# Performance work log

Measured on AMD Instinct MI355X. Metric: run time of the kernel, lower is better.

## Reference

```python
import jax, jax.numpy as jnp
import numpy as np

B, N, K = 128, 1000, 10  # queries, docs per query, NDCG cutoff (hard-coded k=10 in module)


def setup_inputs() -> dict:
    key = jax.random.key(0)
    k1, k2 = jax.random.split(key)
    predictions = jax.random.normal(k1, (B, N), dtype=jnp.float32)
    labels = jax.random.randint(k2, (B, N), 0, 5).astype(jnp.float32)  # graded relevance 0..4
    return {"predictions": predictions, "labels": labels}


def _ndcg_loss(predictions, rel, k=K):
    # relevance gathered in descending-score order, top-k only
    order = jnp.argsort(-predictions, axis=-1)[:, :k]            # [B, k]
    rel_by_score = jnp.take_along_axis(rel, order, axis=-1)      # [B, k]
    ideal_rel, _ = jax.lax.top_k(rel, k)                          # [B, k] sorted desc
    denoms = jnp.log2(jnp.arange(k, dtype=jnp.float32) + 2.0)    # [k]
    dcg = jnp.sum(rel_by_score / denoms, axis=-1)                # [B]
    idcg = jnp.sum(ideal_rel / denoms, axis=-1)                  # [B]
    return jnp.sum(1.0 - dcg / idcg)


def reference(predictions, labels):
    rel = jnp.power(2.0, labels) - 1.0
    return _ndcg_loss(predictions, rel)
```

## Files before the change

kernel.cpp:

```cpp
#include <hip/hip_runtime.h>
#include <stdint.h>

#define B_QUERIES 128
#define N_DOCS    1000
#define K_TOP     10
#define PER_LANE  16

__device__ __forceinline__ uint32_t f32_sortable(float f) {
    uint32_t u = __float_as_uint(f);
    return (u & 0x80000000u) ? ~u : (u | 0x80000000u);
}

__global__ __launch_bounds__(64) void ndcg_row_kernel(
        const float* __restrict__ pred,
        const float* __restrict__ lab,
        float* __restrict__ row_loss) {
    const int row  = blockIdx.x;
    const int lane = threadIdx.x;
    const float* p = pred + row * N_DOCS;
    const float* l = lab  + row * N_DOCS;

    __shared__ int s_lab[N_DOCS];

    const float denom[K_TOP] = {
        1.0f, 1.5849625f, 2.0f, 2.3219281f, 2.5849626f,
        2.8073549f, 3.0f, 3.1699250f, 3.3219281f, 3.4594316f
    };

    uint64_t key[PER_LANE];
    int hist[5] = {0, 0, 0, 0, 0};
    #pragma unroll
    for (int j = 0; j < PER_LANE; ++j) {
        int idx = lane + j * 64;
        if (idx < N_DOCS) {
            float pv = p[idx];
            key[j] = ((uint64_t)f32_sortable(pv) << 32) | (uint32_t)(~idx);
            int lv = (int)(l[idx] + 0.5f);
            s_lab[idx] = lv;
            hist[lv]++;
        } else {
            key[j] = 0;
        }
    }
    __syncthreads();

    #pragma unroll
    for (int v = 0; v < 5; ++v) {
        int h = hist[v];
        #pragma unroll
        for (int off = 32; off > 0; off >>= 1) h += __shfl_xor(h, off, 64);
        hist[v] = h;
    }

    uint64_t lastKey = ~0ull;
    float dcg = 0.0f;
    for (int r = 0; r < K_TOP; ++r) {
        uint64_t best = 0;
        #pragma unroll
        for (int j = 0; j < PER_LANE; ++j) {
            uint64_t k = key[j];
            if (k < lastKey && k > best) best = k;
        }
        #pragma unroll
        for (int off = 32; off > 0; off >>= 1) {
            uint64_t o = (uint64_t)__shfl_xor((unsigned long long)best, off, 64);
            if (o > best) best = o;
        }
        lastKey = best;
        int idx = (int)(~(uint32_t)(best & 0xFFFFFFFFu));
        int lv  = s_lab[idx];
        dcg += (float)((1 << lv) - 1) / denom[r];
    }

    float idcg = 0.0f;
    int pos = 0;
    for (int v = 4; v >= 1; --v) {
        int c = hist[v];
        float rel = (float)((1 << v) - 1);
        for (int t = 0; t < c && pos < K_TOP; ++t) {
            idcg += rel / denom[pos];
            ++pos;
        }
        if (pos >= K_TOP) break;
    }

    if (lane == 0) row_loss[row] = 1.0f - dcg / idcg;
}

__global__ __launch_bounds__(64) void ndcg_reduce_kernel(
        const float* __restrict__ row_loss, float* __restrict__ out) {
    int lane = threadIdx.x;
    float s = row_loss[lane] + row_loss[lane + 64];
    #pragma unroll
    for (int off = 32; off > 0; off >>= 1) s += __shfl_xor(s, off, 64);
    if (lane == 0) out[0] = s;
}

extern "C" void kernel_launch(void* const* d_in, const int* in_sizes, int n_in,
                              void* d_out, int out_size, void* d_ws, size_t ws_size,
                              hipStream_t stream) {
    (void)in_sizes; (void)n_in; (void)out_size; (void)ws_size;
    const float* pred = (const float*)d_in[0];
    const float* lab  = (const float*)d_in[1];
    float* out = (float*)d_out;
    float* ws  = (float*)d_ws;

    ndcg_row_kernel<<<B_QUERIES, 64, 0, stream>>>(pred, lab, ws);
    ndcg_reduce_kernel<<<1, 64, 0, stream>>>(ws, out);
}
```

Baseline: 69.03 us.

## Pack label into sort key, vectorize loads, tree-reduce top-k selection

```diff
diff --git a/kernel.cpp b/kernel.cpp
--- a/kernel.cpp
+++ b/kernel.cpp
@@ -3,12 +3,16 @@
 
 #define B_QUERIES 128
 #define N_DOCS    1000
+#define NVEC      250
 #define K_TOP     10
-#define PER_LANE  16
 
 __device__ __forceinline__ uint32_t f32_sortable(float f) {
     uint32_t u = __float_as_uint(f);
     return (u & 0x80000000u) ? ~u : (u | 0x80000000u);
+}
+
+__device__ __forceinline__ uint64_t u64max(uint64_t a, uint64_t b) {
+    return a > b ? a : b;
 }
 
 __global__ __launch_bounds__(64) void ndcg_row_kernel(
@@ -17,71 +21,78 @@
         float* __restrict__ row_loss) {
     const int row  = blockIdx.x;
     const int lane = threadIdx.x;
-    const float* p = pred + row * N_DOCS;
-    const float* l = lab  + row * N_DOCS;
+    const float4* p4 = (const float4*)(pred + row * N_DOCS);
+    const float4* l4 = (const float4*)(lab  + row * N_DOCS);
 
-    __shared__ int s_lab[N_DOCS];
-
-    const float denom[K_TOP] = {
-        1.0f, 1.5849625f, 2.0f, 2.3219281f, 2.5849626f,
-        2.8073549f, 3.0f, 3.1699250f, 3.3219281f, 3.4594316f
+    const float inv_denom[K_TOP] = {
+        1.0f, 0.63092977f, 0.5f, 0.43067656f, 0.38685282f,
+        0.35620719f, 0.33333334f, 0.31546488f, 0.30102998f, 0.28906483f
     };
 
-    uint64_t key[PER_LANE];
-    int hist[5] = {0, 0, 0, 0, 0};
+    uint64_t key[16];
+    uint64_t h = 0;
+
     #pragma unroll
-    for (int j = 0; j < PER_LANE; ++j) {
-        int idx = lane + j * 64;
-        if (idx < N_DOCS) {
-            float pv = p[idx];
-            key[j] = ((uint64_t)f32_sortable(pv) << 32) | (uint32_t)(~idx);
-            int lv = (int)(l[idx] + 0.5f);
-            s_lab[idx] = lv;
-            hist[lv]++;
-        } else {
-            key[j] = 0;
+    for (int j = 0; j < 4; ++j) {
+        int v = lane + j * 64;
+        bool act = (v < NVEC);
+        float4 pv = act ? p4[v] : make_float4(0.f, 0.f, 0.f, 0.f);
+        float4 lv = act ? l4[v] : make_float4(0.f, 0.f, 0.f, 0.f);
+        float pp[4] = {pv.x, pv.y, pv.z, pv.w};
+        float ll[4] = {lv.x, lv.y, lv.z, lv.w};
+        #pragma unroll
+        for (int c = 0; c < 4; ++c) {
+            int idx = v * 4 + c;
+            int li  = (int)(ll[c] + 0.5f);
+            uint64_t k = ((uint64_t)f32_sortable(pp[c]) << 32)
+                       | ((uint32_t)(1023 - idx) << 8)
+                       | (uint32_t)li;
+            key[j * 4 + c] = act ? k : 0ull;
+            if (act && li > 0) h += 1ull << ((li - 1) * 16);
         }
     }
-    __syncthreads();
 
     #pragma unroll
-    for (int v = 0; v < 5; ++v) {
-        int h = hist[v];
+    for (int off = 32; off > 0; off >>= 1)
+        h += (uint64_t)__shfl_xor((unsigned long long)h, off, 64);
+
+    float idcg = 0.0f;
+    {
+        int pos = 0;
         #pragma unroll
-        for (int off = 32; off > 0; off >>= 1) h += __shfl_xor(h, off, 64);
-        hist[v] = h;
+        for (int v = 4; v >= 1; --v) {
+            int c = (int)((h >> ((v - 1) * 16)) & 0xFFFFull);
+            float rel = (float)((1 << v) - 1);
+            while (c-- > 0 && pos < K_TOP) {
+                idcg += rel * inv_denom[pos];
+                ++pos;
+            }
+            if (pos >= K_TOP) break;
+        }
     }
 
     uint64_t lastKey = ~0ull;
     float dcg = 0.0f;
+    #pragma unroll
     for (int r = 0; r < K_TOP; ++r) {
-        uint64_t best = 0;
+        uint64_t m[16];
         #pragma unroll
-        for (int j = 0; j < PER_LANE; ++j) {
-            uint64_t k = key[j];
-            if (k < lastKey && k > best) best = k;
-        }
+        for (int j = 0; j < 16; ++j)
+            m[j] = (key[j] < lastKey) ? key[j] : 0ull;
+        #pragma unroll
+        for (int s = 8; s > 0; s >>= 1)
+            #pragma unroll
+            for (int j = 0; j < s; ++j)
+                m[j] = u64max(m[j], m[j + s]);
+        uint64_t best = m[0];
         #pragma unroll
         for (int off = 32; off > 0; off >>= 1) {
             uint64_t o = (uint64_t)__shfl_xor((unsigned long long)best, off, 64);
-            if (o > best) best = o;
+            best = u64max(best, o);
         }
         lastKey = best;
-        int idx = (int)(~(uint32_t)(best & 0xFFFFFFFFu));
-        int lv  = s_lab[idx];
-        dcg += (float)((1 << lv) - 1) / denom[r];
-    }
-
-    float idcg = 0.0f;
-    int pos = 0;
-    for (int v = 4; v >= 1; --v) {
-        int c = hist[v];
-        float rel = (float)((1 << v) - 1);
-        for (int t = 0; t < c && pos < K_TOP; ++t) {
-            idcg += rel / denom[pos];
-            ++pos;
-        }
-        if (pos >= K_TOP) break;
+        int lv = (int)(best & 0xFFull);
+        dcg += (float)((1 << lv) - 1) * inv_denom[r];
     }
 
     if (lane == 0) row_loss[row] = 1.0f - dcg / idcg;
```

After: 62.65 us. -9.3%, faster.
